# Performance work log

Hardware: AMD Instinct MI355X
Metric: run time of the kernel (lower is better)

The kernel has to match this reference:

```python
import jax, jax.numpy as jnp
import numpy as np

N = 100000   # nodes
E = 300000   # directed edges
D = 256      # emb_dim
G = 4000     # graphs
L = 5        # num_layer
F_IN = 40    # num_atom_features
NUM_BOND_TYPE = 6       # pretrain-gnns convention; self-loop bond type = 4
NUM_BOND_DIRECTION = 3
EPS = 1e-5


def setup_inputs() -> dict:
    key = jax.random.key(0)
    ks = jax.random.split(key, 32)
    s = 0.05
    inp = {}
    inp["x"] = jax.random.normal(ks[0], (N, F_IN), jnp.float32)
    inp["edge_index"] = jax.random.randint(ks[1], (2, E), 0, N)
    inp["edge_attr"] = jax.random.randint(ks[2], (E, 2), 0, 3)
    inp["batch"] = jnp.sort(jax.random.randint(ks[3], (N,), 0, G))
    # atom embedding (Linear + ReLU)
    inp["embW"] = jax.random.normal(ks[4], (F_IN, D), jnp.float32) * s
    inp["embB"] = jnp.zeros((D,), jnp.float32)
    # per-layer GINConv params (stacked over layers)
    inp["ee1"] = jax.random.normal(ks[5], (L, NUM_BOND_TYPE, D), jnp.float32) * s
    inp["ee2"] = jax.random.normal(ks[6], (L, NUM_BOND_DIRECTION, D), jnp.float32) * s
    inp["W1"] = jax.random.normal(ks[7], (L, D, 2 * D), jnp.float32) * s
    inp["b1"] = jnp.zeros((L, 2 * D), jnp.float32)
    inp["W2"] = jax.random.normal(ks[8], (L, 2 * D, D), jnp.float32) * s
    inp["b2"] = jnp.zeros((L, D), jnp.float32)
    inp["bn_g"] = jnp.ones((L, D), jnp.float32)
    inp["bn_b"] = jnp.zeros((L, D), jnp.float32)
    # MLP head: 256 -> 256 -> 128 -> 64 -> 32 -> 1
    dims = [D, D, D // 2, D // 4, D // 8]
    kk = jax.random.split(ks[9], 5)
    for i in range(4):
        inp[f"hW{i}"] = jax.random.normal(kk[i], (dims[i], dims[i + 1]), jnp.float32) * s
        inp[f"hb{i}"] = jnp.zeros((dims[i + 1],), jnp.float32)
    inp["hWo"] = jax.random.normal(kk[4], (dims[4], 1), jnp.float32) * s
    inp["hbo"] = jnp.zeros((1,), jnp.float32)
    return inp


def reference(x, edge_index, edge_attr, batch, embW, embB, ee1, ee2, W1, b1, W2, b2,
              bn_g, bn_b, hW0, hb0, hW1, hb1, hW2, hb2, hW3, hb3, hWo, hbo):
    src, dst = edge_index[0], edge_index[1]
    ea0, ea1 = edge_attr[:, 0], edge_attr[:, 1]
    # x_embedding1: Linear + ReLU
    h = jax.nn.relu(x @ embW + embB)
    for l in range(L):
        # GINConv: gather source features + edge embeddings, scatter-add to dst
        msg = h[src] + ee1[l][ea0] + ee2[l][ea1]        # [E, D]
        agg = jax.ops.segment_sum(msg, dst, num_segments=N)
        # self-loop message (bond type 4, direction 0)
        agg = agg + h + ee1[l][4] + ee2[l][0]
        # GIN MLP: Linear(D, 2D) -> ReLU -> Linear(2D, D)
        h2 = jax.nn.relu(agg @ W1[l] + b1[l]) @ W2[l] + b2[l]
        # BatchNorm1d (training-mode batch statistics, biased variance)
        mu = h2.mean(axis=0)
        var = h2.var(axis=0)
        h2 = (h2 - mu) * jax.lax.rsqrt(var + EPS) * bn_g[l] + bn_b[l]
        if l < L - 1:
            h2 = jax.nn.relu(h2)
        # dropout with drop_ratio=0.0 -> identity
        h = h2
    # JK == 'last'
    node_rep = h
    # global_mean_pool
    counts = jnp.maximum(jax.ops.segment_sum(jnp.ones((N,), node_rep.dtype), batch, num_segments=G), 1.0)
    mol = jax.ops.segment_sum(node_rep, batch, num_segments=G) / counts[:, None]
    # MLP head
    z = jax.nn.relu(mol @ hW0 + hb0)
    z = jax.nn.relu(z @ hW1 + hb1)
    z = jax.nn.relu(z @ hW2 + hb2)
    z = jax.nn.relu(z @ hW3 + hb3)
    out = z @ hWo + hbo
    return out.reshape(-1)  # MolEmbed.view(-1), num_tasks == 1
```

## Files before the change

kernel.cpp:

```cpp
#include <hip/hip_runtime.h>
#include <hip/hip_bf16.h>

#define NN 100000
#define EE 300000
#define GG 4000
#define LL 5
#define GPB 4
#define SC_CHUNK 1024
#define SC_NB ((NN + SC_CHUNK - 1) / SC_CHUNK)

typedef _Float16 half8  __attribute__((ext_vector_type(8)));
typedef _Float16 half4v __attribute__((ext_vector_type(4)));
typedef float    f32x4  __attribute__((ext_vector_type(4)));

__device__ inline short f2h(float f) {
    _Float16 h = (_Float16)f;
    short s; __builtin_memcpy(&s, &h, 2); return s;
}

__device__ inline void async_load16(const void* g, void* l) {
    __builtin_amdgcn_global_load_lds(
        (const __attribute__((address_space(1))) unsigned int*)g,
        (__attribute__((address_space(3))) unsigned int*)l, 16, 0, 0);
}

__global__ __launch_bounds__(256) void k_count(
    int* __restrict__ deg, const int* __restrict__ ei)
{
    int e = blockIdx.x * 256 + threadIdx.x;
    if (e < EE) atomicAdd(&deg[ei[EE + e]], 1);
}

__global__ __launch_bounds__(256) void k_scan_partial(
    int* __restrict__ partial, const int* __restrict__ deg)
{
    int b = blockIdx.x, t = threadIdx.x;
    int lane = t & 63, w = t >> 6;
    int base = b * SC_CHUNK + t * 4;
    int s = 0;
#pragma unroll
    for (int j = 0; j < 4; ++j) {
        int i = base + j;
        if (i < NN) s += deg[i];
    }
#pragma unroll
    for (int off = 1; off < 64; off <<= 1) s += __shfl_xor(s, off, 64);
    __shared__ int ws[4];
    if (lane == 0) ws[w] = s;
    __syncthreads();
    if (t == 0) partial[b] = ws[0] + ws[1] + ws[2] + ws[3];
}

__global__ __launch_bounds__(128) void k_scan_base(
    int* __restrict__ bases, int* __restrict__ offs, const int* __restrict__ partial)
{
    int t = threadIdx.x;
    int lane = t & 63, w = t >> 6;
    int p = (t < SC_NB) ? partial[t] : 0;
    int x = p;
#pragma unroll
    for (int off = 1; off < 64; off <<= 1) {
        int nb = __shfl_up(x, off, 64);
        if (lane >= off) x += nb;
    }
    __shared__ int w0tot;
    if (t == 63) w0tot = x;
    __syncthreads();
    if (w == 1) x += w0tot;
    if (t < SC_NB) bases[t] = x - p;
    if (t == 0) offs[NN] = EE;
}

__global__ __launch_bounds__(256) void k_scan_final(
    int* __restrict__ offs, int* __restrict__ cursor,
    const int* __restrict__ deg, const int* __restrict__ bases)
{
    int b = blockIdx.x, t = threadIdx.x;
    int lane = t & 63, w = t >> 6;
    int base = b * SC_CHUNK + t * 4;
    int v[4], pre[4], run = 0;
#pragma unroll
    for (int j = 0; j < 4; ++j) {
        int i = base + j;
        v[j] = (i < NN) ? deg[i] : 0;
        pre[j] = run;
        run += v[j];
    }
    int x = run;
#pragma unroll
    for (int off = 1; off < 64; off <<= 1) {
        int nb = __shfl_up(x, off, 64);
        if (lane >= off) x += nb;
    }
    int tex = x - run;
    __shared__ int ws[4];
    if (lane == 63) ws[w] = x;
    __syncthreads();
    int woff = 0;
    for (int k = 0; k < 4; ++k) if (k < w) woff += ws[k];
    int tbase = bases[b] + woff + tex;
#pragma unroll
    for (int j = 0; j < 4; ++j) {
        int i = base + j;
        if (i < NN) { offs[i] = tbase + pre[j]; cursor[i] = tbase + pre[j]; }
    }
}

__global__ __launch_bounds__(256) void k_fill(
    int* __restrict__ csr, int* __restrict__ cursor,
    const int* __restrict__ ei, const int* __restrict__ ea)
{
    int e = blockIdx.x * 256 + threadIdx.x;
    if (e >= EE) return;
    int s = ei[e];
    int d = ei[EE + e];
    int c = ea[2 * e] * 3 + ea[2 * e + 1];
    int slot = atomicAdd(&cursor[d], 1);
    csr[slot] = s | (c << 20);
}

__global__ __launch_bounds__(256) void k_goffs(
    int* __restrict__ goffs, const int* __restrict__ batch)
{
    int n = blockIdx.x * 256 + threadIdx.x;
    if (n >= NN) return;
    int b = batch[n];
    int bp = (n == 0) ? -1 : batch[n - 1];
    for (int g = bp + 1; g <= b; ++g) goffs[g] = n;
    if (n == NN - 1)
        for (int g = b + 1; g <= GG; ++g) goffs[g] = NN;
}

__global__ __launch_bounds__(256) void k_combo(
    float* __restrict__ tbl, const float* __restrict__ ee1, const float* __restrict__ ee2)
{
    int c = blockIdx.x;
    int l = blockIdx.y;
    int t = threadIdx.x;
    int i1 = (c < 9) ? c / 3 : 4;
    int i2 = (c < 9) ? c % 3 : 0;
    tbl[((size_t)l * 10 + c) * 256 + t] =
        ee1[((size_t)l * 6 + i1) * 256 + t] + ee2[((size_t)l * 3 + i2) * 256 + t];
}

__global__ __launch_bounds__(256) void k_pack_emb(
    _Float16* __restrict__ Wep, const float* __restrict__ embW)
{
    int idx = blockIdx.x * 256 + threadIdx.x;
    int ks = idx >> 13, r = idx & 8191;
    int n = r >> 5, kk = r & 31;
    int k = ks * 32 + kk;
    float v = (k < 40) ? embW[(size_t)k * 256 + n] : 0.f;
    Wep[idx] = (_Float16)v;
}

__global__ __launch_bounds__(256) void k_embed_mfma(
    _Float16* __restrict__ H, const float* __restrict__ x,
    const _Float16* __restrict__ Wep, const float* __restrict__ bias)
{
    __shared__ __align__(16) char smem[67584];
    _Float16* As = (_Float16*)smem;
    _Float16* Bs = (_Float16*)(smem + 16384);
    _Float16* Cs = (_Float16*)smem;

    const int t = threadIdx.x;
    const int w = t >> 6, lane = t & 63;
    const int quad = lane >> 4, l16 = lane & 15;
    const int wr = w >> 1, wc = w & 1;
    const int gm0 = blockIdx.x * 128;

#pragma unroll
    for (int i = 0; i < 8; ++i) {
        int u = i * 256 + t;
        async_load16((const char*)Wep + u * 16, (char*)Bs + u * 16);
    }

    {
        int row = t >> 1, half = t & 1;
        int rg = gm0 + row; if (rg > NN - 1) rg = NN - 1;
        const float* xp = x + (size_t)rg * 40 + half * 20;
        float v[20];
#pragma unroll
        for (int j = 0; j < 5; ++j) {
            float4 q = *(const float4*)(xp + j * 4);
            v[j * 4 + 0] = q.x; v[j * 4 + 1] = q.y; v[j * 4 + 2] = q.z; v[j * 4 + 3] = q.w;
        }
#pragma unroll
        for (int j = 0; j < 20; ++j) {
            int col = half * 20 + j;
            int ks = col >> 5, kk = col & 31;
            As[ks * 4096 + row * 32 + kk] = (_Float16)v[j];
        }
        int kb = 8 + half * 12;
#pragma unroll
        for (int j = 0; j < 12; ++j)
            As[4096 + row * 32 + kb + j] = (_Float16)0.f;
    }

    float biasreg[8];
#pragma unroll
    for (int nt = 0; nt < 8; ++nt)
        biasreg[nt] = bias[wc * 128 + nt * 16 + l16];

    f32x4 acc[4][8];
#pragma unroll
    for (int i = 0; i < 4; ++i)
#pragma unroll
        for (int j = 0; j < 8; ++j) acc[i][j] = (f32x4){0.f, 0.f, 0.f, 0.f};

    __syncthreads();

#pragma unroll
    for (int ks = 0; ks < 2; ++ks) {
        half8 af[4], bfr[8];
#pragma unroll
        for (int mt = 0; mt < 4; ++mt)
            af[mt] = *(const half8*)(As + ks * 4096 + (wr * 64 + mt * 16 + l16) * 32 + quad * 8);
#pragma unroll
        for (int nt = 0; nt < 8; ++nt)
            bfr[nt] = *(const half8*)(Bs + ks * 8192 + (wc * 128 + nt * 16 + l16) * 32 + quad * 8);
#pragma unroll
        for (int mt = 0; mt < 4; ++mt)
#pragma unroll
            for (int nt = 0; nt < 8; ++nt)
                acc[mt][nt] = __builtin_amdgcn_mfma_f32_16x16x32_f16(
                    af[mt], bfr[nt], acc[mt][nt], 0, 0, 0);
    }

    __syncthreads();
#pragma unroll
    for (int mt = 0; mt < 4; ++mt)
#pragma unroll
        for (int nt = 0; nt < 8; ++nt)
#pragma unroll
            for (int r = 0; r < 4; ++r) {
                int row = wr * 64 + mt * 16 + quad * 4 + r;
                int col = wc * 128 + nt * 16 + l16;
                Cs[row * 264 + col] = (_Float16)fmaxf(acc[mt][nt][r] + biasreg[nt], 0.f);
            }
    __syncthreads();
#pragma unroll
    for (int i = 0; i < 16; ++i) {
        int u = i * 256 + t;
        int m = u >> 5, ch = u & 31;
        int grow = gm0 + m;
        if (grow < NN)
            *(int4*)(H + (size_t)grow * 256 + ch * 8) =
                *(const int4*)(Cs + m * 264 + ch * 8);
    }
}

template <int AFF>
__global__ __launch_bounds__(256) void k_aggregate(
    _Float16* __restrict__ agg, const _Float16* __restrict__ hin,
    const int* __restrict__ offs, const int* __restrict__ csr,
    const float* __restrict__ tbl,
    const float* __restrict__ scale, const float* __restrict__ shift)
{
    int t = threadIdx.x;
    int w = t >> 6, lane = t & 63;
    int half = lane >> 5, l32 = lane & 31;
    int n = blockIdx.x * 8 + w * 2 + half;
    int ci = l32 * 2;

    const f32x4* tb4 = (const f32x4*)tbl;

    f32x4 sc0, sc1, sh0, sh1;
    if (AFF) {
        sc0 = ((const f32x4*)scale)[ci];  sc1 = ((const f32x4*)scale)[ci + 1];
        sh0 = ((const f32x4*)shift)[ci];  sh1 = ((const f32x4*)shift)[ci + 1];
    }

    half8 hv = *(const half8*)(hin + (size_t)n * 256 + l32 * 8);
    f32x4 a0 = tb4[9 * 64 + ci];
    f32x4 a1 = tb4[9 * 64 + ci + 1];
#pragma unroll
    for (int q = 0; q < 4; ++q) {
        float v0 = (float)hv[q];
        float v1 = (float)hv[4 + q];
        if (AFF) { v0 = fmaf(v0, sc0[q], sh0[q]); v1 = fmaf(v1, sc1[q], sh1[q]); }
        a0[q] += fmaxf(v0, 0.f);
        a1[q] += fmaxf(v1, 0.f);
    }

    int o0 = offs[n], o1 = offs[n + 1];
    for (int e = o0; e < o1; ++e) {
        int entry = csr[e];
        int s = entry & 0xFFFFF;
        int c = entry >> 20;
        half8 gv = *(const half8*)(hin + (size_t)s * 256 + l32 * 8);
        f32x4 t0 = tb4[c * 64 + ci];
        f32x4 t1 = tb4[c * 64 + ci + 1];
#pragma unroll
        for (int q = 0; q < 4; ++q) {
            float v0 = (float)gv[q];
            float v1 = (float)gv[4 + q];
            if (AFF) { v0 = fmaf(v0, sc0[q], sh0[q]); v1 = fmaf(v1, sc1[q], sh1[q]); }
            a0[q] += fmaxf(v0, 0.f) + t0[q];
            a1[q] += fmaxf(v1, 0.f) + t1[q];
        }
    }

    half8 o;
#pragma unroll
    for (int q = 0; q < 4; ++q) {
        o[q]     = (_Float16)a0[q];
        o[4 + q] = (_Float16)a1[q];
    }
    *(half8*)(agg + (size_t)n * 256 + l32 * 8) = o;
}

__global__ __launch_bounds__(256) void k_pack(
    short* __restrict__ dst, const float* __restrict__ src, int K, int Nsz)
{
    int nb = blockIdx.x, kb = blockIdx.y, l = blockIdx.z;
    int t = threadIdx.x;
    __shared__ float T[32][65];
    const float* s = src + ((size_t)l * K + kb * 32) * Nsz + nb * 64;
#pragma unroll
    for (int i = 0; i < 8; ++i) {
        int idx = i * 256 + t;
        int kk = idx >> 6, nl = idx & 63;
        T[kk][nl] = s[(size_t)kk * Nsz + nl];
    }
    __syncthreads();
    int nl = t >> 2, kq = t & 3;
    union { short s[8]; int4 v; } o;
#pragma unroll
    for (int j = 0; j < 8; ++j) o.s[j] = f2h(T[kq * 8 + j][nl]);
    short* d = dst + (((size_t)l * (K / 32) + kb) * Nsz + nb * 64 + nl) * 32 + kq * 8;
    *(int4*)d = o.v;
}

__global__ __launch_bounds__(256, 3) void k_fused_mlp(
    _Float16* __restrict__ H2, const _Float16* __restrict__ A,
    const short* __restrict__ W1p, const float* __restrict__ b1,
    const short* __restrict__ W2p, const float* __restrict__ b2,
    float* __restrict__ stats)
{
    __shared__ __align__(16) char smem[40960];
    _Float16* As = (_Float16*)smem;
    _Float16* Us = (_Float16*)(smem + 32768);
    _Float16* Cs = (_Float16*)smem;

    const int t = threadIdx.x;
    const int w = t >> 6, lane = t & 63;
    const int quad = lane >> 4, l16 = lane & 15;
    const int bm = blockIdx.x;
    const int gm0 = bm * 64;
    const int swz = l16 & 7;

#pragma unroll
    for (int i = 0; i < 8; ++i) {
        int u = i * 256 + t;
        int row = u >> 5;
        int gcol = (u & 31) ^ (row & 7);
        int grow = gm0 + row; if (grow > NN - 1) grow = NN - 1;
        async_load16(A + (size_t)grow * 256 + gcol * 8, (char*)As + u * 16);
    }

    const _Float16* w1w = (const _Float16*)W1p + ((size_t)(w * 16 + l16)) * 32 + quad * 8;
    const _Float16* w2w = (const _Float16*)W2p + ((size_t)(w * 64 + l16)) * 32 + quad * 8;

    half8 w1buf[8];
#pragma unroll
    for (int i = 0; i < 8; ++i)
        w1buf[i] = *(const half8*)(w1w + ((size_t)i * 512) * 32);
    half8 w2k0[4];
#pragma unroll
    for (int nt = 0; nt < 4; ++nt)
        w2k0[nt] = *(const half8*)(w2w + ((size_t)nt * 16) * 32);

    f32x4 acc2[4][4];
#pragma unroll
    for (int i = 0; i < 4; ++i)
#pragma unroll
        for (int j = 0; j < 4; ++j) acc2[i][j] = (f32x4){0.f, 0.f, 0.f, 0.f};

    __syncthreads();

    for (int j = 0; j < 8; ++j) {
        f32x4 acc1[4];
#pragma unroll
        for (int b = 0; b < 4; ++b) acc1[b] = (f32x4){0.f, 0.f, 0.f, 0.f};

#pragma unroll
        for (int kb = 0; kb < 8; ++kb) {
            int slotA = (kb * 4 + quad) ^ swz;
            half8 b1f[4];
#pragma unroll
            for (int urt = 0; urt < 4; ++urt)
                b1f[urt] = *(const half8*)(As + (urt * 16 + l16) * 256 + slotA * 8);
#pragma unroll
            for (int urt = 0; urt < 4; ++urt)
                acc1[urt] = __builtin_amdgcn_mfma_f32_16x16x32_f16(
                    w1buf[kb], b1f[urt], acc1[urt], 0, 0, 0);
        }

        half8 a2n[4];
#pragma unroll
        for (int nt = 0; nt < 4; ++nt)
            a2n[nt] = *(const half8*)(w2w + ((size_t)(j * 2 + 1) * 256 + nt * 16) * 32);

        {
            int ucl = w * 16 + quad * 4;
            float4 bv = *(const float4*)(b1 + j * 64 + ucl);
            int G = ucl >> 3;
            int hs = quad & 1;
#pragma unroll
            for (int urt = 0; urt < 4; ++urt) {
                int ur = urt * 16 + l16;
                int S = G ^ (ur & 7);
                half4v o;
                o[0] = (_Float16)fmaxf(acc1[urt][0] + bv.x, 0.f);
                o[1] = (_Float16)fmaxf(acc1[urt][1] + bv.y, 0.f);
                o[2] = (_Float16)fmaxf(acc1[urt][2] + bv.z, 0.f);
                o[3] = (_Float16)fmaxf(acc1[urt][3] + bv.w, 0.f);
                *(half4v*)(Us + ur * 64 + S * 8 + hs * 4) = o;
            }
        }
        asm volatile("s_waitcnt lgkmcnt(0)" ::: "memory");
        __builtin_amdgcn_s_barrier();
        __builtin_amdgcn_sched_barrier(0);

        if (j < 7) {
#pragma unroll
            for (int i = 0; i < 8; ++i)
                w1buf[i] = *(const half8*)(w1w + ((size_t)i * 512 + (j + 1) * 64) * 32);
        }

        {
            int slotU = quad ^ swz;
            half8 b2f[4];
#pragma unroll
            for (int mt = 0; mt < 4; ++mt)
                b2f[mt] = *(const half8*)(Us + (mt * 16 + l16) * 64 + slotU * 8);
#pragma unroll
            for (int nt = 0; nt < 4; ++nt)
#pragma unroll
                for (int mt = 0; mt < 4; ++mt)
                    acc2[nt][mt] = __builtin_amdgcn_mfma_f32_16x16x32_f16(
                        w2k0[nt], b2f[mt], acc2[nt][mt], 0, 0, 0);
        }
        if (j < 7) {
#pragma unroll
            for (int nt = 0; nt < 4; ++nt)
                w2k0[nt] = *(const half8*)(w2w + ((size_t)(j + 1) * 2 * 256 + nt * 16) * 32);
        }
        {
            int slotU = (4 + quad) ^ swz;
            half8 b2f[4];
#pragma unroll
            for (int mt = 0; mt < 4; ++mt)
                b2f[mt] = *(const half8*)(Us + (mt * 16 + l16) * 64 + slotU * 8);
#pragma unroll
            for (int nt = 0; nt < 4; ++nt)
#pragma unroll
                for (int mt = 0; mt < 4; ++mt)
                    acc2[nt][mt] = __builtin_amdgcn_mfma_f32_16x16x32_f16(
                        a2n[nt], b2f[mt], acc2[nt][mt], 0, 0, 0);
        }
        asm volatile("s_waitcnt lgkmcnt(0)" ::: "memory");
        __builtin_amdgcn_s_barrier();
        __builtin_amdgcn_sched_barrier(0);
    }

    int slot2 = bm & 63;
#pragma unroll
    for (int nt = 0; nt < 4; ++nt) {
        int nb = w * 64 + nt * 16 + quad * 4;
        float4 bv = *(const float4*)(b2 + nb);
        float s1[4] = {0.f, 0.f, 0.f, 0.f};
        float s2[4] = {0.f, 0.f, 0.f, 0.f};
#pragma unroll
        for (int mt = 0; mt < 4; ++mt) {
            int mr = mt * 16 + l16;
            int m = gm0 + mr;
            float v0 = acc2[nt][mt][0] + bv.x;
            float v1 = acc2[nt][mt][1] + bv.y;
            float v2 = acc2[nt][mt][2] + bv.z;
            float v3 = acc2[nt][mt][3] + bv.w;
            half4v o;
            o[0] = (_Float16)v0; o[1] = (_Float16)v1;
            o[2] = (_Float16)v2; o[3] = (_Float16)v3;
            *(half4v*)(Cs + mr * 264 + nb) = o;
            if (m < NN) {
                s1[0] += v0; s1[1] += v1; s1[2] += v2; s1[3] += v3;
                s2[0] += v0 * v0; s2[1] += v1 * v1;
                s2[2] += v2 * v2; s2[3] += v3 * v3;
            }
        }
#pragma unroll
        for (int r = 0; r < 4; ++r) {
            s1[r] += __shfl_xor(s1[r], 1, 64); s2[r] += __shfl_xor(s2[r], 1, 64);
            s1[r] += __shfl_xor(s1[r], 2, 64); s2[r] += __shfl_xor(s2[r], 2, 64);
            s1[r] += __shfl_xor(s1[r], 4, 64); s2[r] += __shfl_xor(s2[r], 4, 64);
            s1[r] += __shfl_xor(s1[r], 8, 64); s2[r] += __shfl_xor(s2[r], 8, 64);
            if (l16 == 0) {
                atomicAdd(&stats[slot2 * 512 + nb + r], s1[r]);
                atomicAdd(&stats[slot2 * 512 + 256 + nb + r], s2[r]);
            }
        }
    }
    __syncthreads();
#pragma unroll
    for (int i = 0; i < 8; ++i) {
        int u = i * 256 + t;
        int m = u >> 5, ch = u & 31;
        int grow = gm0 + m;
        if (grow < NN)
            *(int4*)(H2 + (size_t)grow * 256 + ch * 8) =
                *(const int4*)(Cs + m * 264 + ch * 8);
    }
}

__global__ __launch_bounds__(256) void k_bn_finalize(
    float* __restrict__ scale, float* __restrict__ shift,
    float* __restrict__ stats,
    const float* __restrict__ bn_g, const float* __restrict__ bn_b)
{
    int t = threadIdx.x;
    float s1 = 0.f, s2 = 0.f;
    for (int j = 0; j < 64; ++j) {
        s1 += stats[j * 512 + t];
        s2 += stats[j * 512 + 256 + t];
        stats[j * 512 + t] = 0.f;
        stats[j * 512 + 256 + t] = 0.f;
    }
    float mu  = s1 / (float)NN;
    float var = s2 / (float)NN - mu * mu;
    float sc  = bn_g[t] * rsqrtf(var + 1e-5f);
    scale[t] = sc;
    shift[t] = bn_b[t] - mu * sc;
}

__global__ __launch_bounds__(256) void k_pool(
    float* __restrict__ mol, const _Float16* __restrict__ h,
    const int* __restrict__ goffs,
    const float* __restrict__ scale, const float* __restrict__ shift)
{
    int g = blockIdx.x;
    int t = threadIdx.x;
    int s = goffs[g], e = goffs[g + 1];
    float sum = 0.f;
    for (int n = s; n < e; ++n) sum += (float)h[(size_t)n * 256 + t];
    int c = e - s; if (c < 1) c = 1;
    mol[(size_t)g * 256 + t] = fmaf(sum / (float)c, scale[t], shift[t]);
}

__global__ __launch_bounds__(256) void k_head(
    float* __restrict__ out, const float* __restrict__ mol,
    const float* __restrict__ hW0, const float* __restrict__ hb0,
    const float* __restrict__ hW1, const float* __restrict__ hb1,
    const float* __restrict__ hW2, const float* __restrict__ hb2,
    const float* __restrict__ hW3, const float* __restrict__ hb3,
    const float* __restrict__ hWo, const float* __restrict__ hbo)
{
    __shared__ float za[GPB][256];
    __shared__ float zb[GPB][256];
    const int t = threadIdx.x;
    const int g0 = blockIdx.x * GPB;

#pragma unroll
    for (int g = 0; g < GPB; ++g)
        za[g][t] = mol[(size_t)(g0 + g) * 256 + t];
    __syncthreads();

    {
        float acc[GPB];
#pragma unroll
        for (int g = 0; g < GPB; ++g) acc[g] = 0.f;
        for (int k = 0; k < 256; ++k) {
            float w = hW0[k * 256 + t];
#pragma unroll
            for (int g = 0; g < GPB; ++g) acc[g] = fmaf(za[g][k], w, acc[g]);
        }
        float b = hb0[t];
#pragma unroll
        for (int g = 0; g < GPB; ++g) zb[g][t] = fmaxf(acc[g] + b, 0.f);
    }
    __syncthreads();

    if (t < 128) {
        float acc[GPB];
#pragma unroll
        for (int g = 0; g < GPB; ++g) acc[g] = 0.f;
        for (int k = 0; k < 256; ++k) {
            float w = hW1[k * 128 + t];
#pragma unroll
            for (int g = 0; g < GPB; ++g) acc[g] = fmaf(zb[g][k], w, acc[g]);
        }
        float b = hb1[t];
#pragma unroll
        for (int g = 0; g < GPB; ++g) za[g][t] = fmaxf(acc[g] + b, 0.f);
    }
    __syncthreads();

    if (t < 64) {
        float acc[GPB];
#pragma unroll
        for (int g = 0; g < GPB; ++g) acc[g] = 0.f;
        for (int k = 0; k < 128; ++k) {
            float w = hW2[k * 64 + t];
#pragma unroll
            for (int g = 0; g < GPB; ++g) acc[g] = fmaf(za[g][k], w, acc[g]);
        }
        float b = hb2[t];
#pragma unroll
        for (int g = 0; g < GPB; ++g) zb[g][t] = fmaxf(acc[g] + b, 0.f);
    }
    __syncthreads();

    if (t < 32) {
        float acc[GPB];
#pragma unroll
        for (int g = 0; g < GPB; ++g) acc[g] = 0.f;
        for (int k = 0; k < 64; ++k) {
            float w = hW3[k * 32 + t];
#pragma unroll
            for (int g = 0; g < GPB; ++g) acc[g] = fmaf(zb[g][k], w, acc[g]);
        }
        float b = hb3[t];
#pragma unroll
        for (int g = 0; g < GPB; ++g) za[g][t] = fmaxf(acc[g] + b, 0.f);
    }
    __syncthreads();

    if (t < GPB) {
        float s = hbo[0];
        for (int k = 0; k < 32; ++k) s = fmaf(za[t][k], hWo[k], s);
        out[g0 + t] = s;
    }
}

extern "C" void kernel_launch(void* const* d_in, const int* in_sizes, int n_in,
                              void* d_out, int out_size, void* d_ws, size_t ws_size,
                              hipStream_t stream)
{
    const float* x    = (const float*)d_in[0];
    const int*   ei   = (const int*)d_in[1];
    const int*   ea   = (const int*)d_in[2];
    const int*   batch= (const int*)d_in[3];
    const float* embW = (const float*)d_in[4];
    const float* embB = (const float*)d_in[5];
    const float* ee1  = (const float*)d_in[6];
    const float* ee2  = (const float*)d_in[7];
    const float* W1   = (const float*)d_in[8];
    const float* b1   = (const float*)d_in[9];
    const float* W2   = (const float*)d_in[10];
    const float* b2   = (const float*)d_in[11];
    const float* bng  = (const float*)d_in[12];
    const float* bnb  = (const float*)d_in[13];
    const float* hW0  = (const float*)d_in[14];
    const float* hb0  = (const float*)d_in[15];
    const float* hW1  = (const float*)d_in[16];
    const float* hb1  = (const float*)d_in[17];
    const float* hW2  = (const float*)d_in[18];
    const float* hb2  = (const float*)d_in[19];
    const float* hW3  = (const float*)d_in[20];
    const float* hb3  = (const float*)d_in[21];
    const float* hWo  = (const float*)d_in[22];
    const float* hbo  = (const float*)d_in[23];
    float* out = (float*)d_out;

    char* ws = (char*)d_ws;
    size_t off = 0;
    _Float16* h2buf = (_Float16*)(ws + off); off += (size_t)NN * 256 * 2;
    _Float16* aggbuf= (_Float16*)(ws + off); off += (size_t)NN * 256 * 2;
    short* W1p      = (short*)(ws + off);    off += (size_t)5 * 131072 * 2;
    short* W2p      = (short*)(ws + off);    off += (size_t)5 * 131072 * 2;
    _Float16* Wep   = (_Float16*)(ws + off); off += (size_t)2 * 8192 * 2;
    float* tbl      = (float*)(ws + off);    off += (size_t)5 * 10 * 256 * 4;
    float* stats    = (float*)(ws + off);    off += (size_t)64 * 512 * 4;
    float* scale    = (float*)(ws + off);    off += 256 * 4;
    float* shift    = (float*)(ws + off);    off += 256 * 4;
    float* mol      = (float*)(ws + off);    off += (size_t)GG * 256 * 4;
    int* deg        = (int*)(ws + off);      off += (size_t)NN * 4;
    int* offs       = (int*)(ws + off);      off += (size_t)(NN + 1) * 4;
    int* cursor     = (int*)(ws + off);      off += (size_t)NN * 4;
    int* csr        = (int*)(ws + off);      off += (size_t)EE * 4;
    int* goffs      = (int*)(ws + off);      off += (size_t)(GG + 1) * 4;
    int* partial    = (int*)(ws + off);      off += 128 * 4;
    int* bases      = (int*)(ws + off);      off += 128 * 4;

    hipMemsetAsync(deg, 0, (size_t)NN * 4, stream);
    hipMemsetAsync(stats, 0, (size_t)64 * 512 * 4, stream);
    k_count<<<(EE + 255) / 256, 256, 0, stream>>>(deg, ei);
    k_scan_partial<<<SC_NB, 256, 0, stream>>>(partial, deg);
    k_scan_base<<<1, 128, 0, stream>>>(bases, offs, partial);
    k_scan_final<<<SC_NB, 256, 0, stream>>>(offs, cursor, deg, bases);
    k_fill<<<(EE + 255) / 256, 256, 0, stream>>>(csr, cursor, ei, ea);
    k_goffs<<<(NN + 255) / 256, 256, 0, stream>>>(goffs, batch);
    k_combo<<<dim3(10, 5), 256, 0, stream>>>(tbl, ee1, ee2);
    k_pack<<<dim3(8, 8, 5), 256, 0, stream>>>(W1p, W1, 256, 512);
    k_pack<<<dim3(4, 16, 5), 256, 0, stream>>>(W2p, W2, 512, 256);
    k_pack_emb<<<64, 256, 0, stream>>>(Wep, embW);

    k_embed_mfma<<<782, 256, 0, stream>>>(h2buf, x, Wep, embB);

    const int FB = (NN + 63) / 64;
    for (int l = 0; l < LL; ++l) {
        if (l == 0)
            k_aggregate<0><<<NN / 8, 256, 0, stream>>>(aggbuf, h2buf, offs, csr,
                                                       tbl, scale, shift);
        else
            k_aggregate<1><<<NN / 8, 256, 0, stream>>>(aggbuf, h2buf, offs, csr,
                                                       tbl + (size_t)l * 10 * 256, scale, shift);
        k_fused_mlp<<<FB, 256, 0, stream>>>(h2buf, aggbuf,
                                            W1p + (size_t)l * 131072, b1 + l * 512,
                                            W2p + (size_t)l * 131072, b2 + l * 256, stats);
        k_bn_finalize<<<1, 256, 0, stream>>>(scale, shift, stats, bng + l * 256, bnb + l * 256);
    }

    k_pool<<<GG, 256, 0, stream>>>(mol, h2buf, goffs, scale, shift);
    k_head<<<GG / GPB, 256, 0, stream>>>(out, mol,
                                         hW0, hb0, hW1, hb1, hW2, hb2, hW3, hb3, hWo, hbo);
}
```

Measured before the change: 914.1 us.

## Merge setup kernels, fold BN finalize into MLP, double-buffer U tile

Merges the goffs, combo-table, weight-packing, embedding-pack and buffer-zeroing work into one prologue kernel, which replaces several launches and two memsets. The per-layer BN finalize kernel is removed: the last block of the fused MLP, found through an atomic ticket, reduces the stats and writes scale and shift. The intermediate U tile in shared memory is double-buffered so the per-iteration barrier can be dropped. This raises LDS use and relies on correct fencing around the last-block pattern.

```diff
diff --git a/kernel.cpp b/kernel.cpp
--- a/kernel.cpp
+++ b/kernel.cpp
@@ -119,39 +119,73 @@
     csr[slot] = s | (c << 20);
 }
 
-__global__ __launch_bounds__(256) void k_goffs(
-    int* __restrict__ goffs, const int* __restrict__ batch)
-{
-    int n = blockIdx.x * 256 + threadIdx.x;
-    if (n >= NN) return;
-    int b = batch[n];
-    int bp = (n == 0) ? -1 : batch[n - 1];
-    for (int g = bp + 1; g <= b; ++g) goffs[g] = n;
-    if (n == NN - 1)
-        for (int g = b + 1; g <= GG; ++g) goffs[g] = NN;
-}
-
-__global__ __launch_bounds__(256) void k_combo(
-    float* __restrict__ tbl, const float* __restrict__ ee1, const float* __restrict__ ee2)
-{
-    int c = blockIdx.x;
-    int l = blockIdx.y;
-    int t = threadIdx.x;
-    int i1 = (c < 9) ? c / 3 : 4;
-    int i2 = (c < 9) ? c % 3 : 0;
-    tbl[((size_t)l * 10 + c) * 256 + t] =
-        ee1[((size_t)l * 6 + i1) * 256 + t] + ee2[((size_t)l * 3 + i2) * 256 + t];
-}
-
-__global__ __launch_bounds__(256) void k_pack_emb(
-    _Float16* __restrict__ Wep, const float* __restrict__ embW)
-{
-    int idx = blockIdx.x * 256 + threadIdx.x;
-    int ks = idx >> 13, r = idx & 8191;
-    int n = r >> 5, kk = r & 31;
-    int k = ks * 32 + kk;
-    float v = (k < 40) ? embW[(size_t)k * 256 + n] : 0.f;
-    Wep[idx] = (_Float16)v;
+__device__ __forceinline__ void pack_body(
+    short* __restrict__ dst, const float* __restrict__ src, int K, int Nsz,
+    int nb, int kb, int l, int t, float (*T)[65])
+{
+    const float* s = src + ((size_t)l * K + kb * 32) * Nsz + nb * 64;
+#pragma unroll
+    for (int i = 0; i < 8; ++i) {
+        int idx = i * 256 + t;
+        int kk = idx >> 6, nl = idx & 63;
+        T[kk][nl] = s[(size_t)kk * Nsz + nl];
+    }
+    __syncthreads();
+    int nl = t >> 2, kq = t & 3;
+    union { short s[8]; int4 v; } o;
+#pragma unroll
+    for (int j = 0; j < 8; ++j) o.s[j] = f2h(T[kq * 8 + j][nl]);
+    short* d = dst + (((size_t)l * (K / 32) + kb) * Nsz + nb * 64 + nl) * 32 + kq * 8;
+    *(int4*)d = o.v;
+}
+
+__global__ __launch_bounds__(256) void k_prologue(
+    int* __restrict__ goffs, const int* __restrict__ batch,
+    float* __restrict__ tbl, const float* __restrict__ ee1, const float* __restrict__ ee2,
+    short* __restrict__ W1p, const float* __restrict__ W1,
+    short* __restrict__ W2p, const float* __restrict__ W2,
+    _Float16* __restrict__ Wep, const float* __restrict__ embW,
+    int* __restrict__ deg, float* __restrict__ stats, unsigned* __restrict__ ticket)
+{
+    __shared__ float T[32][65];
+    int b = blockIdx.x, t = threadIdx.x;
+    if (b < 391) {
+        int n = b * 256 + t;
+        if (n >= NN) return;
+        int bb = batch[n];
+        int bp = (n == 0) ? -1 : batch[n - 1];
+        for (int g = bp + 1; g <= bb; ++g) goffs[g] = n;
+        if (n == NN - 1)
+            for (int g = bb + 1; g <= GG; ++g) goffs[g] = NN;
+    } else if (b < 441) {
+        int idx = b - 391;
+        int c = idx % 10, l = idx / 10;
+        int i1 = (c < 9) ? c / 3 : 4;
+        int i2 = (c < 9) ? c % 3 : 0;
+        tbl[((size_t)l * 10 + c) * 256 + t] =
+            ee1[((size_t)l * 6 + i1) * 256 + t] + ee2[((size_t)l * 3 + i2) * 256 + t];
+    } else if (b < 761) {
+        int idx = b - 441;
+        pack_body(W1p, W1, 256, 512, idx & 7, (idx >> 3) & 7, idx >> 6, t, T);
+    } else if (b < 1081) {
+        int idx = b - 761;
+        pack_body(W2p, W2, 512, 256, idx & 3, (idx >> 2) & 15, idx >> 6, t, T);
+    } else if (b < 1145) {
+        int idx = (b - 1081) * 256 + t;
+        int ks = idx >> 13, r = idx & 8191;
+        int n = r >> 5, kk = r & 31;
+        int k = ks * 32 + kk;
+        float v = (k < 40) ? embW[(size_t)k * 256 + n] : 0.f;
+        Wep[idx] = (_Float16)v;
+    } else if (b < 1536) {
+        int n = (b - 1145) * 256 + t;
+        if (n < NN) deg[n] = 0;
+    } else {
+        int gi = (b - 1536) * 1024 + t * 4;
+        float4 z = {0.f, 0.f, 0.f, 0.f};
+        *(float4*)(stats + gi) = z;
+        if (b == 1536 && t == 0) *ticket = 0u;
+    }
 }
 
 __global__ __launch_bounds__(256) void k_embed_mfma(
@@ -310,38 +344,20 @@
     *(half8*)(agg + (size_t)n * 256 + l32 * 8) = o;
 }
 
-__global__ __launch_bounds__(256) void k_pack(
-    short* __restrict__ dst, const float* __restrict__ src, int K, int Nsz)
-{
-    int nb = blockIdx.x, kb = blockIdx.y, l = blockIdx.z;
-    int t = threadIdx.x;
-    __shared__ float T[32][65];
-    const float* s = src + ((size_t)l * K + kb * 32) * Nsz + nb * 64;
-#pragma unroll
-    for (int i = 0; i < 8; ++i) {
-        int idx = i * 256 + t;
-        int kk = idx >> 6, nl = idx & 63;
-        T[kk][nl] = s[(size_t)kk * Nsz + nl];
-    }
-    __syncthreads();
-    int nl = t >> 2, kq = t & 3;
-    union { short s[8]; int4 v; } o;
-#pragma unroll
-    for (int j = 0; j < 8; ++j) o.s[j] = f2h(T[kq * 8 + j][nl]);
-    short* d = dst + (((size_t)l * (K / 32) + kb) * Nsz + nb * 64 + nl) * 32 + kq * 8;
-    *(int4*)d = o.v;
-}
-
 __global__ __launch_bounds__(256, 3) void k_fused_mlp(
     _Float16* __restrict__ H2, const _Float16* __restrict__ A,
     const short* __restrict__ W1p, const float* __restrict__ b1,
     const short* __restrict__ W2p, const float* __restrict__ b2,
-    float* __restrict__ stats)
-{
-    __shared__ __align__(16) char smem[40960];
+    float* __restrict__ stats,
+    float* __restrict__ scale, float* __restrict__ shift,
+    const float* __restrict__ bn_g, const float* __restrict__ bn_b,
+    unsigned* __restrict__ ticket)
+{
+    __shared__ __align__(16) char smem[49152];
     _Float16* As = (_Float16*)smem;
-    _Float16* Us = (_Float16*)(smem + 32768);
+    _Float16* UsB = (_Float16*)(smem + 32768);
     _Float16* Cs = (_Float16*)smem;
+    __shared__ int lastflag;
 
     const int t = threadIdx.x;
     const int w = t >> 6, lane = t & 63;
@@ -380,6 +396,7 @@
     __syncthreads();
 
     for (int j = 0; j < 8; ++j) {
+        _Float16* Us = UsB + (j & 1) * 4096;
         f32x4 acc1[4];
 #pragma unroll
         for (int b = 0; b < 4; ++b) acc1[b] = (f32x4){0.f, 0.f, 0.f, 0.f};
@@ -460,9 +477,6 @@
                     acc2[nt][mt] = __builtin_amdgcn_mfma_f32_16x16x32_f16(
                         a2n[nt], b2f[mt], acc2[nt][mt], 0, 0, 0);
         }
-        asm volatile("s_waitcnt lgkmcnt(0)" ::: "memory");
-        __builtin_amdgcn_s_barrier();
-        __builtin_amdgcn_sched_barrier(0);
     }
 
     int slot2 = bm & 63;
@@ -512,26 +526,34 @@
             *(int4*)(H2 + (size_t)grow * 256 + ch * 8) =
                 *(const int4*)(Cs + m * 264 + ch * 8);
     }
-}
-
-__global__ __launch_bounds__(256) void k_bn_finalize(
-    float* __restrict__ scale, float* __restrict__ shift,
-    float* __restrict__ stats,
-    const float* __restrict__ bn_g, const float* __restrict__ bn_b)
-{
-    int t = threadIdx.x;
-    float s1 = 0.f, s2 = 0.f;
-    for (int j = 0; j < 64; ++j) {
-        s1 += stats[j * 512 + t];
-        s2 += stats[j * 512 + 256 + t];
-        stats[j * 512 + t] = 0.f;
-        stats[j * 512 + 256 + t] = 0.f;
-    }
-    float mu  = s1 / (float)NN;
-    float var = s2 / (float)NN - mu * mu;
-    float sc  = bn_g[t] * rsqrtf(var + 1e-5f);
-    scale[t] = sc;
-    shift[t] = bn_b[t] - mu * sc;
+
+    __threadfence();
+    __syncthreads();
+    if (t == 0) {
+        unsigned old = atomicAdd(ticket, 1u);
+        lastflag = (old == gridDim.x - 1) ? 1 : 0;
+    }
+    __syncthreads();
+    if (lastflag) {
+        __threadfence();
+        float s1 = 0.f, s2 = 0.f;
+        for (int jj = 0; jj < 64; ++jj) {
+            s1 += __hip_atomic_load(&stats[jj * 512 + t],
+                                    __ATOMIC_RELAXED, __HIP_MEMORY_SCOPE_AGENT);
+            s2 += __hip_atomic_load(&stats[jj * 512 + 256 + t],
+                                    __ATOMIC_RELAXED, __HIP_MEMORY_SCOPE_AGENT);
+            __hip_atomic_store(&stats[jj * 512 + t], 0.f,
+                               __ATOMIC_RELAXED, __HIP_MEMORY_SCOPE_AGENT);
+            __hip_atomic_store(&stats[jj * 512 + 256 + t], 0.f,
+                               __ATOMIC_RELAXED, __HIP_MEMORY_SCOPE_AGENT);
+        }
+        float mu  = s1 / (float)NN;
+        float var = s2 / (float)NN - mu * mu;
+        float scv = bn_g[t] * rsqrtf(var + 1e-5f);
+        scale[t] = scv;
+        shift[t] = bn_b[t] - mu * scv;
+        if (t == 0) *ticket = 0u;
+    }
 }
 
 __global__ __launch_bounds__(256) void k_pool(
@@ -682,19 +704,16 @@
     int* goffs      = (int*)(ws + off);      off += (size_t)(GG + 1) * 4;
     int* partial    = (int*)(ws + off);      off += 128 * 4;
     int* bases      = (int*)(ws + off);      off += 128 * 4;
-
-    hipMemsetAsync(deg, 0, (size_t)NN * 4, stream);
-    hipMemsetAsync(stats, 0, (size_t)64 * 512 * 4, stream);
+    unsigned* ticket= (unsigned*)(ws + off); off += 4;
+
+    k_prologue<<<1568, 256, 0, stream>>>(goffs, batch, tbl, ee1, ee2,
+                                         W1p, W1, W2p, W2, Wep, embW,
+                                         deg, stats, ticket);
     k_count<<<(EE + 255) / 256, 256, 0, stream>>>(deg, ei);
     k_scan_partial<<<SC_NB, 256, 0, stream>>>(partial, deg);
     k_scan_base<<<1, 128, 0, stream>>>(bases, offs, partial);
     k_scan_final<<<SC_NB, 256, 0, stream>>>(offs, cursor, deg, bases);
     k_fill<<<(EE + 255) / 256, 256, 0, stream>>>(csr, cursor, ei, ea);
-    k_goffs<<<(NN + 255) / 256, 256, 0, stream>>>(goffs, batch);
-    k_combo<<<dim3(10, 5), 256, 0, stream>>>(tbl, ee1, ee2);
-    k_pack<<<dim3(8, 8, 5), 256, 0, stream>>>(W1p, W1, 256, 512);
-    k_pack<<<dim3(4, 16, 5), 256, 0, stream>>>(W2p, W2, 512, 256);
-    k_pack_emb<<<64, 256, 0, stream>>>(Wep, embW);
 
     k_embed_mfma<<<782, 256, 0, stream>>>(h2buf, x, Wep, embB);
 
@@ -708,8 +727,9 @@
                                                        tbl + (size_t)l * 10 * 256, scale, shift);
         k_fused_mlp<<<FB, 256, 0, stream>>>(h2buf, aggbuf,
                                             W1p + (size_t)l * 131072, b1 + l * 512,
-                                            W2p + (size_t)l * 131072, b2 + l * 256, stats);
-        k_bn_finalize<<<1, 256, 0, stream>>>(scale, shift, stats, bng + l * 256, bnb + l * 256);
+                                            W2p + (size_t)l * 131072, b2 + l * 256,
+                                            stats, scale, shift,
+                                            bng + l * 256, bnb + l * 256, ticket);
     }
 
     k_pool<<<GG, 256, 0, stream>>>(mol, h2buf, goffs, scale, shift);
```

Measured after the change: 1.883 ms. +106.0%, slower.
